# Performance work log

Measured on AMD Instinct MI355X. Metric: run time of the kernel, lower is better.

The kernel has to match this reference:

```python
import jax, jax.numpy as jnp
import numpy as np
import math

D_MODEL = 1024
NUM_HEADS = 16
D_K = D_MODEL // NUM_HEADS
B, L = 2, 2048


def setup_inputs() -> dict:
    key = jax.random.key(0)
    ks = jax.random.split(key, 9)
    s = 1.0 / math.sqrt(D_MODEL)
    inp = {
        "x": jax.random.normal(ks[0], (B, L, D_MODEL), dtype=jnp.float32),
        "mask": jnp.ones((B, L), dtype=jnp.int32),
        "Wq": jax.random.uniform(ks[1], (D_MODEL, D_MODEL), jnp.float32, -s, s),
        "bq": jax.random.uniform(ks[2], (D_MODEL,), jnp.float32, -s, s),
        "Wk": jax.random.uniform(ks[3], (D_MODEL, D_MODEL), jnp.float32, -s, s),
        "bk": jax.random.uniform(ks[4], (D_MODEL,), jnp.float32, -s, s),
        "Wv": jax.random.uniform(ks[5], (D_MODEL, D_MODEL), jnp.float32, -s, s),
        "bv": jax.random.uniform(ks[6], (D_MODEL,), jnp.float32, -s, s),
        "Wo": jax.random.uniform(ks[7], (D_MODEL, D_MODEL), jnp.float32, -s, s),
        "bo": jax.random.uniform(ks[8], (D_MODEL,), jnp.float32, -s, s),
    }
    return inp


def reference(x, mask, Wq, bq, Wk, bk, Wv, bv, Wo, bo):
    b, l, _ = x.shape
    def proj(W, bias):
        # nn.Linear: x @ W.T + b, then split heads -> [B, H, L, d_k]
        y = x @ W.T + bias
        return y.reshape(b, l, NUM_HEADS, D_K).transpose(0, 2, 1, 3)
    Q, K, V = proj(Wq, bq), proj(Wk, bk), proj(Wv, bv)
    scores = jnp.einsum("bhqd,bhkd->bhqk", Q, K) / math.sqrt(D_K)
    # mask: [B, L] -> [B, 1, 1, L]; fill masked positions with -1e9
    m = mask[:, None, None, :]
    scores = jnp.where(m == 0, jnp.float32(-1e9), scores)
    attn = jax.nn.softmax(scores, axis=-1)
    out = jnp.einsum("bhqk,bhkd->bhqd", attn, V)
    out = out.transpose(0, 2, 1, 3).reshape(b, l, D_MODEL)
    return out @ Wo.T + bo, attn
```

## Files before the change

### kernel.cpp

```cpp
#include <hip/hip_runtime.h>

#define D_MODEL 1024
#define NHEADS  16
#define DKH     64
#define BATCH   2
#define SEQ     2048
#define MTOT    (BATCH*SEQ)
#define NQKV    (3*D_MODEL)
#define LDT     72
#define LDPF    68

typedef __bf16 bf16x8 __attribute__((ext_vector_type(8)));
typedef float  f32x4  __attribute__((ext_vector_type(4)));
typedef unsigned short u16x8 __attribute__((ext_vector_type(8)));
typedef unsigned short u16x4 __attribute__((ext_vector_type(4)));

#define MFMA(a,b,c) __builtin_amdgcn_mfma_f32_16x16x32_bf16(a,b,c,0,0,0)

#if __has_builtin(__builtin_amdgcn_exp2f)
#define EXP2(x) __builtin_amdgcn_exp2f(x)
#else
#define EXP2(x) exp2f(x)
#endif

#define GLOAD_LDS16(g, l) __builtin_amdgcn_global_load_lds( \
    (const __attribute__((address_space(1))) unsigned int*)(g), \
    (__attribute__((address_space(3))) unsigned int*)(l), 16, 0, 0)

__device__ __forceinline__ unsigned short f2bf(float f) {
  unsigned u = __builtin_bit_cast(unsigned, f);
  u += 0x7fffu + ((u >> 16) & 1u);
  return (unsigned short)(u >> 16);
}

__device__ __forceinline__ bf16x8 ldfrag(const unsigned short* p) {
  return __builtin_bit_cast(bf16x8, *(const u16x8*)p);
}

__device__ __forceinline__ bf16x8 ldswz(const unsigned short* tile, int row, int chunk) {
  return ldfrag(tile + row*64 + ((chunk ^ (row & 7)) << 3));
}

__device__ __forceinline__ void stage_tile(const unsigned short* __restrict__ gbase,
                                           size_t row_stride_us,
                                           unsigned short* lds_tile, int tid) {
#pragma unroll
  for (int it = 0; it < 2; ++it) {
    int chunk = it*256 + tid;
    int row = chunk >> 3, c = chunk & 7;
    int sc  = c ^ (row & 7);
    GLOAD_LDS16(gbase + (size_t)row*row_stride_us + sc*8, lds_tile + chunk*8);
  }
}

__global__ __launch_bounds__(256) void cvt_kernel(const float* __restrict__ src,
                                                  unsigned short* __restrict__ dst, int n4) {
  int i = blockIdx.x * blockDim.x + threadIdx.x;
  if (i >= n4) return;
  float4 f = ((const float4*)src)[i];
  u16x4 o;
  o[0] = f2bf(f.x); o[1] = f2bf(f.y); o[2] = f2bf(f.z); o[3] = f2bf(f.w);
  ((u16x4*)dst)[i] = o;
}

__global__ __launch_bounds__(256) void mask_kernel(const int* __restrict__ m,
                                                   float* __restrict__ mf, int n) {
  int i = blockIdx.x * blockDim.x + threadIdx.x;
  if (i < n) mf[i] = m[i] ? 0.0f : -1e9f;
}

__global__ __launch_bounds__(256) void qkv_gemm(const unsigned short* __restrict__ xbf,
                                                const unsigned short* __restrict__ wbf,
                                                const float* __restrict__ bq,
                                                const float* __restrict__ bk,
                                                const float* __restrict__ bv,
                                                unsigned short* __restrict__ Qo,
                                                unsigned short* __restrict__ Ko,
                                                unsigned short* __restrict__ VTo)
{
  __shared__ __attribute__((aligned(16))) unsigned short As[64*LDT];
  __shared__ __attribute__((aligned(16))) unsigned short Bs[64*LDT];
  const int tid  = threadIdx.x;
  const int wid  = tid >> 6;
  const int lane = tid & 63;
  const int lr   = lane & 15;
  const int lg   = lane >> 4;
  const int m0   = blockIdx.x * 64;
  const int n0   = blockIdx.y * 64;

  f32x4 zero = {0.f, 0.f, 0.f, 0.f};
  f32x4 acc[4];
  acc[0] = zero; acc[1] = zero; acc[2] = zero; acc[3] = zero;

  const int ko = lg * 8;
  for (int kt = 0; kt < D_MODEL/64; ++kt) {
    __syncthreads();
    for (int v = tid; v < 512; v += 256) {
      int row = v >> 3, c8 = (v & 7) * 8;
      *(u16x8*)&As[row*LDT + c8] = *(const u16x8*)&xbf[(size_t)(m0+row)*D_MODEL + kt*64 + c8];
      *(u16x8*)&Bs[row*LDT + c8] = *(const u16x8*)&wbf[(size_t)(n0+row)*D_MODEL + kt*64 + c8];
    }
    __syncthreads();
    bf16x8 a0 = ldfrag(&As[(wid*16+lr)*LDT + ko]);
    bf16x8 a1 = ldfrag(&As[(wid*16+lr)*LDT + 32 + ko]);
#pragma unroll
    for (int ct = 0; ct < 4; ++ct) {
      bf16x8 b0 = ldfrag(&Bs[(ct*16+lr)*LDT + ko]);
      bf16x8 b1 = ldfrag(&Bs[(ct*16+lr)*LDT + 32 + ko]);
      acc[ct] = MFMA(a0, b0, acc[ct]);
      acc[ct] = MFMA(a1, b1, acc[ct]);
    }
  }

  const int proj = n0 >> 10;
  const int rem0 = n0 & 1023;
  const int h    = rem0 >> 6;
  const float* bias = (proj == 0) ? bq : (proj == 1) ? bk : bv;

  if (proj < 2) {
    unsigned short* dst = (proj == 0) ? Qo : Ko;
#pragma unroll
    for (int ct = 0; ct < 4; ++ct) {
      int col = ct*16 + lr;
      float bval = bias[rem0 + col];
#pragma unroll
      for (int r = 0; r < 4; ++r) {
        int m  = m0 + wid*16 + lg*4 + r;
        int b_ = m >> 11, lq = m & (SEQ-1);
        dst[((size_t)((b_*NHEADS + h)*SEQ + lq))*DKH + col] = f2bf(acc[ct][r] + bval);
      }
    }
  } else {
    __syncthreads();
#pragma unroll
    for (int ct = 0; ct < 4; ++ct) {
      int col = ct*16 + lr;
      float bval = bias[rem0 + col];
#pragma unroll
      for (int r = 0; r < 4; ++r) {
        int row = wid*16 + lg*4 + r;
        As[col*LDT + row] = f2bf(acc[ct][r] + bval);
      }
    }
    __syncthreads();
    int b_ = m0 >> 11, lq0 = m0 & (SEQ-1);
    int bh = b_*NHEADS + h;
    for (int v = tid; v < 512; v += 256) {
      int dk = v >> 3, c8 = (v & 7) * 8;
      *(u16x8*)&VTo[((size_t)(bh*DKH + dk))*SEQ + lq0 + c8] = *(const u16x8*)&As[dk*LDT + c8];
    }
  }
}

__global__ __launch_bounds__(256) void attn_kernel(const unsigned short* __restrict__ Qw,
                                                   const unsigned short* __restrict__ Kw,
                                                   const unsigned short* __restrict__ VTw,
                                                   const float* __restrict__ maskf,
                                                   float* __restrict__ attn_out,
                                                   unsigned short* __restrict__ OH)
{
  __shared__ __attribute__((aligned(16))) unsigned short Ks[2][64*64];
  __shared__ __attribute__((aligned(16))) unsigned short Vs[2][64*64];
  __shared__ __attribute__((aligned(16))) float Pf[4][16*LDPF];

  const int tid  = threadIdx.x;
  const int wid  = tid >> 6;
  const int lane = tid & 63;
  const int lr   = lane & 15;
  const int lg   = lane >> 4;
  const int q0   = blockIdx.x * 64;
  const int bh   = blockIdx.y;
  const int b_   = bh >> 4;
  const int h    = bh & 15;

  const unsigned short* Qb = Qw  + (size_t)bh*SEQ*DKH;
  const unsigned short* Kb = Kw  + (size_t)bh*SEQ*DKH;
  const unsigned short* Vb = VTw + (size_t)bh*DKH*SEQ;
  const f32x4* mf4 = (const f32x4*)(maskf + b_*SEQ);

  const int qrow = q0 + wid*16 + lr;
  bf16x8 aq0 = ldfrag(&Qb[(size_t)qrow*DKH + lg*8]);
  bf16x8 aq1 = ldfrag(&Qb[(size_t)qrow*DKH + 32 + lg*8]);

  const float c2 = 0.18033688011112042f;
  f32x4 zero = {0.f, 0.f, 0.f, 0.f};

  float lsum = 0.f;
  stage_tile(Kb, DKH, Ks[0], tid);
  __syncthreads();
  for (int kt = 0; kt < SEQ/64; ++kt) {
    int cur = kt & 1;
    if (kt < SEQ/64 - 1)
      stage_tile(Kb + (size_t)(kt+1)*64*DKH, DKH, Ks[cur^1], tid);
#pragma unroll
    for (int ct = 0; ct < 4; ++ct) {
      int row = ct*16 + lr;
      bf16x8 k0 = ldswz(Ks[cur], row, lg);
      bf16x8 k1 = ldswz(Ks[cur], row, lg + 4);
      f32x4 acc = zero;
      acc = MFMA(k0, aq0, acc);
      acc = MFMA(k1, aq1, acc);
      f32x4 md = mf4[kt*16 + ct*4 + lg];
#pragma unroll
      for (int r = 0; r < 4; ++r)
        lsum += EXP2(__builtin_fmaf(acc[r], c2, md[r]));
    }
    __syncthreads();
  }
  lsum += __shfl_xor(lsum, 16);
  lsum += __shfl_xor(lsum, 32);
  const float il = 1.0f / lsum;

  f32x4 oacc[4];
  oacc[0] = zero; oacc[1] = zero; oacc[2] = zero; oacc[3] = zero;

  float* PfW = Pf[wid];
  float* arow0 = attn_out + ((size_t)bh*SEQ + q0 + wid*16)*SEQ;

  stage_tile(Kb, DKH, Ks[0], tid);
  stage_tile(Vb, SEQ, Vs[0], tid);
  __syncthreads();
  for (int kt = 0; kt < SEQ/64; ++kt) {
    int cur = kt & 1;
    if (kt < SEQ/64 - 1) {
      stage_tile(Kb + (size_t)(kt+1)*64*DKH, DKH, Ks[cur^1], tid);
      stage_tile(Vb + (size_t)(kt+1)*64,     SEQ, Vs[cur^1], tid);
    }
#pragma unroll
    for (int ct = 0; ct < 4; ++ct) {
      int row = ct*16 + lr;
      bf16x8 k0 = ldswz(Ks[cur], row, lg);
      bf16x8 k1 = ldswz(Ks[cur], row, lg + 4);
      f32x4 acc = zero;
      acc = MFMA(k0, aq0, acc);
      acc = MFMA(k1, aq1, acc);
      f32x4 md = mf4[kt*16 + ct*4 + lg];
      f32x4 av;
#pragma unroll
      for (int r = 0; r < 4; ++r)
        av[r] = EXP2(__builtin_fmaf(acc[r], c2, md[r])) * il;
      *(f32x4*)&PfW[lr*LDPF + ct*16 + lg*4] = av;
    }
#pragma unroll
    for (int i = 0; i < 4; ++i) {
      int r16 = i*4 + lg;
      f32x4 v = *(const f32x4*)&PfW[r16*LDPF + lr*4];
      *(f32x4*)(arow0 + (size_t)r16*SEQ + kt*64 + lr*4) = v;
    }
    {
      const float* pp = &PfW[lr*LDPF];
      f32x4 p0 = *(const f32x4*)(pp + lg*8);
      f32x4 p1 = *(const f32x4*)(pp + lg*8 + 4);
      f32x4 p2 = *(const f32x4*)(pp + 32 + lg*8);
      f32x4 p3 = *(const f32x4*)(pp + 32 + lg*8 + 4);
      u16x8 w0, w1;
#pragma unroll
      for (int j = 0; j < 4; ++j) {
        w0[j]   = f2bf(p0[j]); w0[j+4] = f2bf(p1[j]);
        w1[j]   = f2bf(p2[j]); w1[j+4] = f2bf(p3[j]);
      }
      bf16x8 pa0 = __builtin_bit_cast(bf16x8, w0);
      bf16x8 pa1 = __builtin_bit_cast(bf16x8, w1);
#pragma unroll
      for (int ct = 0; ct < 4; ++ct) {
        int row = ct*16 + lr;
        bf16x8 v0 = ldswz(Vs[cur], row, lg);
        bf16x8 v1 = ldswz(Vs[cur], row, lg + 4);
        oacc[ct] = MFMA(pa0, v0, oacc[ct]);
        oacc[ct] = MFMA(pa1, v1, oacc[ct]);
      }
    }
    __syncthreads();
  }

#pragma unroll
  for (int ct = 0; ct < 4; ++ct) {
    int dk = ct*16 + lr;
#pragma unroll
    for (int r = 0; r < 4; ++r) {
      int q = q0 + wid*16 + lg*4 + r;
      OH[(size_t)(b_*SEQ + q)*D_MODEL + h*DKH + dk] = f2bf(oacc[ct][r]);
    }
  }
}

__global__ __launch_bounds__(256) void out_gemm(const unsigned short* __restrict__ OH,
                                                const unsigned short* __restrict__ wo,
                                                const float* __restrict__ bo,
                                                float* __restrict__ out)
{
  __shared__ __attribute__((aligned(16))) unsigned short As[64*LDT];
  __shared__ __attribute__((aligned(16))) unsigned short Bs[64*LDT];
  const int tid  = threadIdx.x;
  const int wid  = tid >> 6;
  const int lane = tid & 63;
  const int lr   = lane & 15;
  const int lg   = lane >> 4;
  const int m0   = blockIdx.x * 64;
  const int n0   = blockIdx.y * 64;

  f32x4 zero = {0.f, 0.f, 0.f, 0.f};
  f32x4 acc[4];
  acc[0] = zero; acc[1] = zero; acc[2] = zero; acc[3] = zero;

  const int ko = lg * 8;
  for (int kt = 0; kt < D_MODEL/64; ++kt) {
    __syncthreads();
    for (int v = tid; v < 512; v += 256) {
      int row = v >> 3, c8 = (v & 7) * 8;
      *(u16x8*)&As[row*LDT + c8] = *(const u16x8*)&OH[(size_t)(m0+row)*D_MODEL + kt*64 + c8];
      *(u16x8*)&Bs[row*LDT + c8] = *(const u16x8*)&wo[(size_t)(n0+row)*D_MODEL + kt*64 + c8];
    }
    __syncthreads();
    bf16x8 a0 = ldfrag(&As[(wid*16+lr)*LDT + ko]);
    bf16x8 a1 = ldfrag(&As[(wid*16+lr)*LDT + 32 + ko]);
#pragma unroll
    for (int ct = 0; ct < 4; ++ct) {
      bf16x8 b0 = ldfrag(&Bs[(ct*16+lr)*LDT + ko]);
      bf16x8 b1 = ldfrag(&Bs[(ct*16+lr)*LDT + 32 + ko]);
      acc[ct] = MFMA(a0, b0, acc[ct]);
      acc[ct] = MFMA(a1, b1, acc[ct]);
    }
  }
#pragma unroll
  for (int ct = 0; ct < 4; ++ct) {
    int n = n0 + ct*16 + lr;
    float bval = bo[n];
#pragma unroll
    for (int r = 0; r < 4; ++r) {
      int m = m0 + wid*16 + lg*4 + r;
      out[(size_t)m*D_MODEL + n] = acc[ct][r] + bval;
    }
  }
}

extern "C" void kernel_launch(void* const* d_in, const int* in_sizes, int n_in,
                              void* d_out, int out_size, void* d_ws, size_t ws_size,
                              hipStream_t stream) {
  const float* x    = (const float*)d_in[0];
  const int*   mask = (const int*)  d_in[1];
  const float* Wq   = (const float*)d_in[2];
  const float* bq   = (const float*)d_in[3];
  const float* Wk   = (const float*)d_in[4];
  const float* bk   = (const float*)d_in[5];
  const float* Wv   = (const float*)d_in[6];
  const float* bv   = (const float*)d_in[7];
  const float* Wo   = (const float*)d_in[8];
  const float* bo   = (const float*)d_in[9];

  float* out0 = (float*)d_out;
  float* attn = out0 + (size_t)MTOT * D_MODEL;

  unsigned short* ws   = (unsigned short*)d_ws;
  unsigned short* xbf  = ws;
  unsigned short* wqkv = xbf  + (size_t)MTOT * D_MODEL;
  unsigned short* wob  = wqkv + (size_t)NQKV * D_MODEL;
  unsigned short* Qw   = wob  + (size_t)D_MODEL * D_MODEL;
  unsigned short* Kw   = Qw   + (size_t)MTOT * D_MODEL;
  unsigned short* VTw  = Kw   + (size_t)MTOT * D_MODEL;
  unsigned short* OH   = VTw  + (size_t)MTOT * D_MODEL;

  float* maskf = (float*)xbf;

  cvt_kernel<<<4096, 256, 0, stream>>>(x,  xbf, MTOT*D_MODEL/4);
  cvt_kernel<<<1024, 256, 0, stream>>>(Wq, wqkv,                 D_MODEL*D_MODEL/4);
  cvt_kernel<<<1024, 256, 0, stream>>>(Wk, wqkv +   D_MODEL*D_MODEL, D_MODEL*D_MODEL/4);
  cvt_kernel<<<1024, 256, 0, stream>>>(Wv, wqkv + 2*D_MODEL*D_MODEL, D_MODEL*D_MODEL/4);
  cvt_kernel<<<1024, 256, 0, stream>>>(Wo, wob, D_MODEL*D_MODEL/4);

  qkv_gemm<<<dim3(MTOT/64, NQKV/64), 256, 0, stream>>>(xbf, wqkv, bq, bk, bv, Qw, Kw, VTw);
  mask_kernel<<<16, 256, 0, stream>>>(mask, maskf, BATCH*SEQ);
  attn_kernel<<<dim3(SEQ/64, BATCH*NHEADS), 256, 0, stream>>>(Qw, Kw, VTw, maskf, attn, OH);
  out_gemm<<<dim3(MTOT/64, D_MODEL/64), 256, 0, stream>>>(OH, wob, bo, out0);
}
```

Baseline: 802.4 us.

## Use 128x128 LDS-swizzled GEMM tiles, remap attention blocks, nontemporal attn stores

Replaces the 64x64 GEMMs for the QKV and output projections with a shared 128x128 tile routine. It uses direct global-to-LDS loads with XOR swizzling and a 2x2 wave layout, which gives more MFMA work per load, and the QKV epilogue now writes through swizzled LDS as vectorized stores. The attention kernel remaps its block index so that heads are interleaved across blocks, and it writes the attention matrix in two 32-column chunks through a swizzled LDS buffer using nontemporal stores. It also raises wave priority around the PV MFMAs. The float-to-bf16 conversion now uses a native cast, and the GEMM grids shrink to a quarter of their former block count, which may reduce occupancy.

Measured after the change: 688.1 us. 14.2% less time.

```diff
diff --git a/kernel.cpp b/kernel.cpp
--- a/kernel.cpp
+++ b/kernel.cpp
@@ -7,8 +7,6 @@
 #define SEQ     2048
 #define MTOT    (BATCH*SEQ)
 #define NQKV    (3*D_MODEL)
-#define LDT     72
-#define LDPF    68
 
 typedef __bf16 bf16x8 __attribute__((ext_vector_type(8)));
 typedef float  f32x4  __attribute__((ext_vector_type(4)));
@@ -28,9 +26,8 @@
     (__attribute__((address_space(3))) unsigned int*)(l), 16, 0, 0)
 
 __device__ __forceinline__ unsigned short f2bf(float f) {
-  unsigned u = __builtin_bit_cast(unsigned, f);
-  u += 0x7fffu + ((u >> 16) & 1u);
-  return (unsigned short)(u >> 16);
+  __bf16 h = (__bf16)f;
+  return __builtin_bit_cast(unsigned short, h);
 }
 
 __device__ __forceinline__ bf16x8 ldfrag(const unsigned short* p) {
@@ -67,6 +64,50 @@
                                                    float* __restrict__ mf, int n) {
   int i = blockIdx.x * blockDim.x + threadIdx.x;
   if (i < n) mf[i] = m[i] ? 0.0f : -1e9f;
+}
+
+__device__ __forceinline__ void gemm128_bt(const unsigned short* __restrict__ A,
+                                           const unsigned short* __restrict__ B,
+                                           unsigned short* SB,
+                                           int m0, int n0, int tid,
+                                           f32x4 (&acc)[4][4])
+{
+  unsigned short* As = SB;
+  unsigned short* Bs = SB + 8192;
+  const int lane = tid & 63;
+  const int lr   = lane & 15;
+  const int lg   = lane >> 4;
+  const int wid  = tid >> 6;
+  const int wr   = wid >> 1;
+  const int wc   = wid & 1;
+
+  for (int kt = 0; kt < D_MODEL/64; ++kt) {
+    __syncthreads();
+#pragma unroll
+    for (int it = 0; it < 4; ++it) {
+      int chunk = it*256 + tid;
+      int row = chunk >> 3, c = chunk & 7, sc = c ^ (row & 7);
+      GLOAD_LDS16(A + (size_t)(m0+row)*D_MODEL + kt*64 + sc*8, As + chunk*8);
+      GLOAD_LDS16(B + (size_t)(n0+row)*D_MODEL + kt*64 + sc*8, Bs + chunk*8);
+    }
+    __syncthreads();
+    bf16x8 a[4][2], b[4][2];
+#pragma unroll
+    for (int i = 0; i < 4; ++i) {
+      int ra = wr*64 + i*16 + lr;
+      int rb = wc*64 + i*16 + lr;
+      a[i][0] = ldswz(As, ra, lg);  a[i][1] = ldswz(As, ra, lg + 4);
+      b[i][0] = ldswz(Bs, rb, lg);  b[i][1] = ldswz(Bs, rb, lg + 4);
+    }
+#pragma unroll
+    for (int i = 0; i < 4; ++i)
+#pragma unroll
+      for (int j = 0; j < 4; ++j) {
+        acc[i][j] = MFMA(a[i][0], b[j][0], acc[i][j]);
+        acc[i][j] = MFMA(a[i][1], b[j][1], acc[i][j]);
+      }
+  }
+  __syncthreads();
 }
 
 __global__ __launch_bounds__(256) void qkv_gemm(const unsigned short* __restrict__ xbf,
@@ -78,76 +119,74 @@
                                                 unsigned short* __restrict__ Ko,
                                                 unsigned short* __restrict__ VTo)
 {
-  __shared__ __attribute__((aligned(16))) unsigned short As[64*LDT];
-  __shared__ __attribute__((aligned(16))) unsigned short Bs[64*LDT];
+  __shared__ __attribute__((aligned(16))) unsigned short SB[16384];
   const int tid  = threadIdx.x;
-  const int wid  = tid >> 6;
-  const int lane = tid & 63;
-  const int lr   = lane & 15;
-  const int lg   = lane >> 4;
-  const int m0   = blockIdx.x * 64;
-  const int n0   = blockIdx.y * 64;
-
-  f32x4 zero = {0.f, 0.f, 0.f, 0.f};
-  f32x4 acc[4];
-  acc[0] = zero; acc[1] = zero; acc[2] = zero; acc[3] = zero;
-
-  const int ko = lg * 8;
-  for (int kt = 0; kt < D_MODEL/64; ++kt) {
-    __syncthreads();
-    for (int v = tid; v < 512; v += 256) {
-      int row = v >> 3, c8 = (v & 7) * 8;
-      *(u16x8*)&As[row*LDT + c8] = *(const u16x8*)&xbf[(size_t)(m0+row)*D_MODEL + kt*64 + c8];
-      *(u16x8*)&Bs[row*LDT + c8] = *(const u16x8*)&wbf[(size_t)(n0+row)*D_MODEL + kt*64 + c8];
-    }
-    __syncthreads();
-    bf16x8 a0 = ldfrag(&As[(wid*16+lr)*LDT + ko]);
-    bf16x8 a1 = ldfrag(&As[(wid*16+lr)*LDT + 32 + ko]);
-#pragma unroll
-    for (int ct = 0; ct < 4; ++ct) {
-      bf16x8 b0 = ldfrag(&Bs[(ct*16+lr)*LDT + ko]);
-      bf16x8 b1 = ldfrag(&Bs[(ct*16+lr)*LDT + 32 + ko]);
-      acc[ct] = MFMA(a0, b0, acc[ct]);
-      acc[ct] = MFMA(a1, b1, acc[ct]);
-    }
-  }
-
-  const int proj = n0 >> 10;
-  const int rem0 = n0 & 1023;
-  const int h    = rem0 >> 6;
+  const int lane = tid & 63, lr = lane & 15, lg = lane >> 4;
+  const int wid  = tid >> 6, wr = wid >> 1, wc = wid & 1;
+  const int m0   = blockIdx.x * 128;
+  const int n0   = blockIdx.y * 128;
+
+  f32x4 acc[4][4];
+#pragma unroll
+  for (int i = 0; i < 4; ++i)
+#pragma unroll
+    for (int j = 0; j < 4; ++j) acc[i][j] = f32x4{0.f,0.f,0.f,0.f};
+
+  gemm128_bt(xbf, wbf, SB, m0, n0, tid, acc);
+
+  const int proj  = n0 >> 10;
+  const int rem0  = n0 & 1023;
+  const int hbase = rem0 >> 6;
+  const int b_    = m0 >> 11;
+  const int lq0   = m0 & (SEQ-1);
   const float* bias = (proj == 0) ? bq : (proj == 1) ? bk : bv;
 
   if (proj < 2) {
     unsigned short* dst = (proj == 0) ? Qo : Ko;
 #pragma unroll
-    for (int ct = 0; ct < 4; ++ct) {
-      int col = ct*16 + lr;
-      float bval = bias[rem0 + col];
-#pragma unroll
-      for (int r = 0; r < 4; ++r) {
-        int m  = m0 + wid*16 + lg*4 + r;
-        int b_ = m >> 11, lq = m & (SEQ-1);
-        dst[((size_t)((b_*NHEADS + h)*SEQ + lq))*DKH + col] = f2bf(acc[ct][r] + bval);
-      }
+    for (int i = 0; i < 4; ++i)
+#pragma unroll
+      for (int j = 0; j < 4; ++j) {
+        int col = wc*64 + j*16 + lr;
+        float bval = bias[rem0 + col];
+        int slot = col >> 3, ce = col & 7;
+#pragma unroll
+        for (int r = 0; r < 4; ++r) {
+          int row = wr*64 + i*16 + lg*4 + r;
+          SB[row*128 + ((slot ^ (row & 15)) << 3) + ce] = f2bf(acc[i][j][r] + bval);
+        }
+      }
+    __syncthreads();
+#pragma unroll
+    for (int it = 0; it < 8; ++it) {
+      int v = it*256 + tid;
+      int row = v >> 4, slot = v & 15;
+      u16x8 val = *(const u16x8*)&SB[row*128 + ((slot ^ (row & 15)) << 3)];
+      int h = hbase + (slot >> 3), dk8 = (slot & 7)*8;
+      int lq = lq0 + row;
+      *(u16x8*)&dst[((size_t)((b_*NHEADS + h)*SEQ + lq))*DKH + dk8] = val;
     }
   } else {
-    __syncthreads();
-#pragma unroll
-    for (int ct = 0; ct < 4; ++ct) {
-      int col = ct*16 + lr;
-      float bval = bias[rem0 + col];
-#pragma unroll
-      for (int r = 0; r < 4; ++r) {
-        int row = wid*16 + lg*4 + r;
-        As[col*LDT + row] = f2bf(acc[ct][r] + bval);
-      }
-    }
-    __syncthreads();
-    int b_ = m0 >> 11, lq0 = m0 & (SEQ-1);
-    int bh = b_*NHEADS + h;
-    for (int v = tid; v < 512; v += 256) {
-      int dk = v >> 3, c8 = (v & 7) * 8;
-      *(u16x8*)&VTo[((size_t)(bh*DKH + dk))*SEQ + lq0 + c8] = *(const u16x8*)&As[dk*LDT + c8];
+#pragma unroll
+    for (int i = 0; i < 4; ++i)
+#pragma unroll
+      for (int j = 0; j < 4; ++j) {
+        int c = wc*64 + j*16 + lr;
+        float bval = bias[rem0 + c];
+#pragma unroll
+        for (int r = 0; r < 4; ++r) {
+          int lq = wr*64 + i*16 + lg*4 + r;
+          SB[c*128 + (((lq >> 3) ^ (c & 15)) << 3) + (lq & 7)] = f2bf(acc[i][j][r] + bval);
+        }
+      }
+    __syncthreads();
+#pragma unroll
+    for (int it = 0; it < 8; ++it) {
+      int v = it*256 + tid;
+      int c = v >> 4, s = v & 15;
+      u16x8 val = *(const u16x8*)&SB[c*128 + ((s ^ (c & 15)) << 3)];
+      int bh = b_*NHEADS + hbase + (c >> 6), dk = c & 63;
+      *(u16x8*)&VTo[((size_t)(bh*DKH + dk))*SEQ + lq0 + s*8] = val;
     }
   }
 }
@@ -159,17 +198,23 @@
                                                    float* __restrict__ attn_out,
                                                    unsigned short* __restrict__ OH)
 {
-  __shared__ __attribute__((aligned(16))) unsigned short Ks[2][64*64];
-  __shared__ __attribute__((aligned(16))) unsigned short Vs[2][64*64];
-  __shared__ __attribute__((aligned(16))) float Pf[4][16*LDPF];
+  __shared__ __attribute__((aligned(16))) unsigned short S[20480];
+  unsigned short* K0 = S;
+  unsigned short* K1 = S + 4096;
+  unsigned short* V0 = S + 8192;
+  unsigned short* V1 = S + 12288;
+  float* Pf = (float*)(S + 16384);
 
   const int tid  = threadIdx.x;
   const int wid  = tid >> 6;
   const int lane = tid & 63;
   const int lr   = lane & 15;
   const int lg   = lane >> 4;
-  const int q0   = blockIdx.x * 64;
-  const int bh   = blockIdx.y;
+
+  const int flat = blockIdx.y * gridDim.x + blockIdx.x;
+  const int nf   = (flat & 7)*128 + (flat >> 3);
+  const int q0   = (nf & 31) * 64;
+  const int bh   = nf >> 5;
   const int b_   = bh >> 4;
   const int h    = bh & 15;
 
@@ -182,28 +227,29 @@
   bf16x8 aq0 = ldfrag(&Qb[(size_t)qrow*DKH + lg*8]);
   bf16x8 aq1 = ldfrag(&Qb[(size_t)qrow*DKH + 32 + lg*8]);
 
-  const float c2 = 0.18033688011112042f;
+  const float SCL = 0.18033688011112042f;
   f32x4 zero = {0.f, 0.f, 0.f, 0.f};
 
   float lsum = 0.f;
-  stage_tile(Kb, DKH, Ks[0], tid);
+  stage_tile(Kb, DKH, K0, tid);
   __syncthreads();
   for (int kt = 0; kt < SEQ/64; ++kt) {
-    int cur = kt & 1;
+    unsigned short* cur = (kt & 1) ? K1 : K0;
+    unsigned short* nxt = (kt & 1) ? K0 : K1;
     if (kt < SEQ/64 - 1)
-      stage_tile(Kb + (size_t)(kt+1)*64*DKH, DKH, Ks[cur^1], tid);
+      stage_tile(Kb + (size_t)(kt+1)*64*DKH, DKH, nxt, tid);
 #pragma unroll
     for (int ct = 0; ct < 4; ++ct) {
       int row = ct*16 + lr;
-      bf16x8 k0 = ldswz(Ks[cur], row, lg);
-      bf16x8 k1 = ldswz(Ks[cur], row, lg + 4);
+      bf16x8 k0 = ldswz(cur, row, lg);
+      bf16x8 k1 = ldswz(cur, row, lg + 4);
       f32x4 acc = zero;
       acc = MFMA(k0, aq0, acc);
       acc = MFMA(k1, aq1, acc);
       f32x4 md = mf4[kt*16 + ct*4 + lg];
 #pragma unroll
       for (int r = 0; r < 4; ++r)
-        lsum += EXP2(__builtin_fmaf(acc[r], c2, md[r]));
+        lsum += EXP2(__builtin_fmaf(acc[r], SCL, md[r]));
     }
     __syncthreads();
   }
@@ -214,62 +260,64 @@
   f32x4 oacc[4];
   oacc[0] = zero; oacc[1] = zero; oacc[2] = zero; oacc[3] = zero;
 
-  float* PfW = Pf[wid];
+  float* PfW = Pf + wid*512;
   float* arow0 = attn_out + ((size_t)bh*SEQ + q0 + wid*16)*SEQ;
 
-  stage_tile(Kb, DKH, Ks[0], tid);
-  stage_tile(Vb, SEQ, Vs[0], tid);
+  stage_tile(Kb, DKH, K0, tid);
+  stage_tile(Vb, SEQ, V0, tid);
   __syncthreads();
   for (int kt = 0; kt < SEQ/64; ++kt) {
-    int cur = kt & 1;
+    unsigned short* Kc = (kt & 1) ? K1 : K0;
+    unsigned short* Kn = (kt & 1) ? K0 : K1;
+    unsigned short* Vc = (kt & 1) ? V1 : V0;
+    unsigned short* Vn = (kt & 1) ? V0 : V1;
     if (kt < SEQ/64 - 1) {
-      stage_tile(Kb + (size_t)(kt+1)*64*DKH, DKH, Ks[cur^1], tid);
-      stage_tile(Vb + (size_t)(kt+1)*64,     SEQ, Vs[cur^1], tid);
-    }
+      stage_tile(Kb + (size_t)(kt+1)*64*DKH, DKH, Kn, tid);
+      stage_tile(Vb + (size_t)(kt+1)*64,     SEQ, Vn, tid);
+    }
+    bf16x8 pa0, pa1;
+#pragma unroll
+    for (int ch = 0; ch < 2; ++ch) {
+#pragma unroll
+      for (int c2 = 0; c2 < 2; ++c2) {
+        int ct = ch*2 + c2;
+        int row = ct*16 + lr;
+        bf16x8 k0 = ldswz(Kc, row, lg);
+        bf16x8 k1 = ldswz(Kc, row, lg + 4);
+        f32x4 acc = zero;
+        acc = MFMA(k0, aq0, acc);
+        acc = MFMA(k1, aq1, acc);
+        f32x4 md = mf4[kt*16 + ct*4 + lg];
+        f32x4 av;
+#pragma unroll
+        for (int r = 0; r < 4; ++r)
+          av[r] = EXP2(__builtin_fmaf(acc[r], SCL, md[r])) * il;
+        *(f32x4*)&PfW[lr*32 + (((c2*4 + lg) ^ (lr & 7)) << 2)] = av;
+      }
+#pragma unroll
+      for (int i = 0; i < 2; ++i) {
+        int row = i*8 + (lane >> 3), cs = lane & 7;
+        f32x4 v = *(const f32x4*)&PfW[row*32 + ((cs ^ (row & 7)) << 2)];
+        __builtin_nontemporal_store(v,
+            (f32x4*)(arow0 + (size_t)row*SEQ + kt*64 + ch*32 + cs*4));
+      }
+      f32x4 r0 = *(const f32x4*)&PfW[lr*32 + (((lg*2    ) ^ (lr & 7)) << 2)];
+      f32x4 r1 = *(const f32x4*)&PfW[lr*32 + (((lg*2 + 1) ^ (lr & 7)) << 2)];
+      bf16x8 pa;
+#pragma unroll
+      for (int j = 0; j < 4; ++j) { pa[j] = (__bf16)r0[j]; pa[j+4] = (__bf16)r1[j]; }
+      if (ch == 0) pa0 = pa; else pa1 = pa;
+    }
+    __builtin_amdgcn_s_setprio(1);
 #pragma unroll
     for (int ct = 0; ct < 4; ++ct) {
       int row = ct*16 + lr;
-      bf16x8 k0 = ldswz(Ks[cur], row, lg);
-      bf16x8 k1 = ldswz(Ks[cur], row, lg + 4);
-      f32x4 acc = zero;
-      acc = MFMA(k0, aq0, acc);
-      acc = MFMA(k1, aq1, acc);
-      f32x4 md = mf4[kt*16 + ct*4 + lg];
-      f32x4 av;
-#pragma unroll
-      for (int r = 0; r < 4; ++r)
-        av[r] = EXP2(__builtin_fmaf(acc[r], c2, md[r])) * il;
-      *(f32x4*)&PfW[lr*LDPF + ct*16 + lg*4] = av;
-    }
-#pragma unroll
-    for (int i = 0; i < 4; ++i) {
-      int r16 = i*4 + lg;
-      f32x4 v = *(const f32x4*)&PfW[r16*LDPF + lr*4];
-      *(f32x4*)(arow0 + (size_t)r16*SEQ + kt*64 + lr*4) = v;
-    }
-    {
-      const float* pp = &PfW[lr*LDPF];
-      f32x4 p0 = *(const f32x4*)(pp + lg*8);
-      f32x4 p1 = *(const f32x4*)(pp + lg*8 + 4);
-      f32x4 p2 = *(const f32x4*)(pp + 32 + lg*8);
-      f32x4 p3 = *(const f32x4*)(pp + 32 + lg*8 + 4);
-      u16x8 w0, w1;
-#pragma unroll
-      for (int j = 0; j < 4; ++j) {
-        w0[j]   = f2bf(p0[j]); w0[j+4] = f2bf(p1[j]);
-        w1[j]   = f2bf(p2[j]); w1[j+4] = f2bf(p3[j]);
-      }
-      bf16x8 pa0 = __builtin_bit_cast(bf16x8, w0);
-      bf16x8 pa1 = __builtin_bit_cast(bf16x8, w1);
-#pragma unroll
-      for (int ct = 0; ct < 4; ++ct) {
-        int row = ct*16 + lr;
-        bf16x8 v0 = ldswz(Vs[cur], row, lg);
-        bf16x8 v1 = ldswz(Vs[cur], row, lg + 4);
-        oacc[ct] = MFMA(pa0, v0, oacc[ct]);
-        oacc[ct] = MFMA(pa1, v1, oacc[ct]);
-      }
-    }
+      bf16x8 v0 = ldswz(Vc, row, lg);
+      bf16x8 v1 = ldswz(Vc, row, lg + 4);
+      oacc[ct] = MFMA(pa0, v0, oacc[ct]);
+      oacc[ct] = MFMA(pa1, v1, oacc[ct]);
+    }
+    __builtin_amdgcn_s_setprio(0);
     __syncthreads();
   }
 
@@ -289,49 +337,33 @@
                                                 const float* __restrict__ bo,
                                                 float* __restrict__ out)
 {
-  __shared__ __attribute__((aligned(16))) unsigned short As[64*LDT];
-  __shared__ __attribute__((aligned(16))) unsigned short Bs[64*LDT];
+  __shared__ __attribute__((aligned(16))) unsigned short SB[16384];
   const int tid  = threadIdx.x;
-  const int wid  = tid >> 6;
-  const int lane = tid & 63;
-  const int lr   = lane & 15;
-  const int lg   = lane >> 4;
-  const int m0   = blockIdx.x * 64;
-  const int n0   = blockIdx.y * 64;
-
-  f32x4 zero = {0.f, 0.f, 0.f, 0.f};
-  f32x4 acc[4];
-  acc[0] = zero; acc[1] = zero; acc[2] = zero; acc[3] = zero;
-
-  const int ko = lg * 8;
-  for (int kt = 0; kt < D_MODEL/64; ++kt) {
-    __syncthreads();
-    for (int v = tid; v < 512; v += 256) {
-      int row = v >> 3, c8 = (v & 7) * 8;
-      *(u16x8*)&As[row*LDT + c8] = *(const u16x8*)&OH[(size_t)(m0+row)*D_MODEL + kt*64 + c8];
-      *(u16x8*)&Bs[row*LDT + c8] = *(const u16x8*)&wo[(size_t)(n0+row)*D_MODEL + kt*64 + c8];
-    }
-    __syncthreads();
-    bf16x8 a0 = ldfrag(&As[(wid*16+lr)*LDT + ko]);
-    bf16x8 a1 = ldfrag(&As[(wid*16+lr)*LDT + 32 + ko]);
-#pragma unroll
-    for (int ct = 0; ct < 4; ++ct) {
-      bf16x8 b0 = ldfrag(&Bs[(ct*16+lr)*LDT + ko]);
-      bf16x8 b1 = ldfrag(&Bs[(ct*16+lr)*LDT + 32 + ko]);
-      acc[ct] = MFMA(a0, b0, acc[ct]);
-      acc[ct] = MFMA(a1, b1, acc[ct]);
-    }
-  }
-#pragma unroll
-  for (int ct = 0; ct < 4; ++ct) {
-    int n = n0 + ct*16 + lr;
-    float bval = bo[n];
-#pragma unroll
-    for (int r = 0; r < 4; ++r) {
-      int m = m0 + wid*16 + lg*4 + r;
-      out[(size_t)m*D_MODEL + n] = acc[ct][r] + bval;
-    }
-  }
+  const int lane = tid & 63, lr = lane & 15, lg = lane >> 4;
+  const int wid  = tid >> 6, wr = wid >> 1, wc = wid & 1;
+  const int m0   = blockIdx.x * 128;
+  const int n0   = blockIdx.y * 128;
+
+  f32x4 acc[4][4];
+#pragma unroll
+  for (int i = 0; i < 4; ++i)
+#pragma unroll
+    for (int j = 0; j < 4; ++j) acc[i][j] = f32x4{0.f,0.f,0.f,0.f};
+
+  gemm128_bt(OH, wo, SB, m0, n0, tid, acc);
+
+#pragma unroll
+  for (int i = 0; i < 4; ++i)
+#pragma unroll
+    for (int j = 0; j < 4; ++j) {
+      int n = n0 + wc*64 + j*16 + lr;
+      float bval = bo[n];
+#pragma unroll
+      for (int r = 0; r < 4; ++r) {
+        int m = m0 + wr*64 + i*16 + lg*4 + r;
+        out[(size_t)m*D_MODEL + n] = acc[i][j][r] + bval;
+      }
+    }
 }
 
 extern "C" void kernel_launch(void* const* d_in, const int* in_sizes, int n_in,
@@ -368,8 +400,8 @@
   cvt_kernel<<<1024, 256, 0, stream>>>(Wv, wqkv + 2*D_MODEL*D_MODEL, D_MODEL*D_MODEL/4);
   cvt_kernel<<<1024, 256, 0, stream>>>(Wo, wob, D_MODEL*D_MODEL/4);
 
-  qkv_gemm<<<dim3(MTOT/64, NQKV/64), 256, 0, stream>>>(xbf, wqkv, bq, bk, bv, Qw, Kw, VTw);
+  qkv_gemm<<<dim3(MTOT/128, NQKV/128), 256, 0, stream>>>(xbf, wqkv, bq, bk, bv, Qw, Kw, VTw);
   mask_kernel<<<16, 256, 0, stream>>>(mask, maskf, BATCH*SEQ);
   attn_kernel<<<dim3(SEQ/64, BATCH*NHEADS), 256, 0, stream>>>(Qw, Kw, VTw, maskf, attn, OH);
-  out_gemm<<<dim3(MTOT/64, D_MODEL/64), 256, 0, stream>>>(OH, wob, bo, out0);
-}
+  out_gemm<<<dim3(MTOT/128, D_MODEL/128), 256, 0, stream>>>(OH, wob, bo, out0);
+}
```
